# Performance work log

Hardware: AMD Instinct MI355X
Metric: run time of the kernel (lower is better)

Reference implementation:

```python
import jax, jax.numpy as jnp
import numpy as np

D = 2048          # hidden_size
N = 16            # num query heads
K = 8             # num kv heads
G = N // K        # GQA groups
H = 128           # head_dim (== head_dim_original, already padded)
T_NOISE = 1024
T_PAD = 1024
MAX_KV = 4096
THETA = 1000000.0
EPS = 1e-6
SM_SCALE = H ** -0.5
NEG = -1e30


def apply_rope(x, pos):
    # x: (T, heads, H); rotate-half (NeoX/Qwen) convention over full head_dim
    half = H // 2
    inv_freq = 1.0 / (THETA ** (jnp.arange(half, dtype=jnp.float32) / half))
    ang = pos.astype(jnp.float32)[:, None] * inv_freq[None, :]      # (T, half)
    cos = jnp.cos(ang)[:, None, :]
    sin = jnp.sin(ang)[:, None, :]
    x1, x2 = x[..., :half], x[..., half:]
    return jnp.concatenate([x1 * cos - x2 * sin, x2 * cos + x1 * sin], axis=-1)


def rms_norm(x, scale):
    var = jnp.mean(jnp.square(x), axis=-1, keepdims=True)
    return x * jax.lax.rsqrt(var + EPS) * scale


def setup_inputs() -> dict:
    key = jax.random.key(0)
    ks = jax.random.split(key, 10)
    cache_len = 1024
    actual_ctx = 768
    u = lambda k, shape: jax.random.uniform(k, shape, jnp.float32) * 0.01  # nnx uniform init
    return {
        "x_noise": jax.random.normal(ks[0], (T_NOISE, D), jnp.float32),
        "target_hidden": jax.random.normal(ks[1], (T_PAD, D), jnp.float32),
        "noise_positions": jnp.arange(T_NOISE, dtype=jnp.int32) + cache_len + actual_ctx,
        "ctx_positions": jnp.arange(T_PAD, dtype=jnp.int32) + cache_len,
        "kv_cache_k": jax.random.normal(ks[2], (1, N, MAX_KV, H), jnp.float32),
        "kv_cache_v": jax.random.normal(ks[3], (1, N, MAX_KV, H), jnp.float32),
        "cache_len": cache_len,
        "actual_ctx_count": actual_ctx,
        "Wq": u(ks[4], (D, N, H)),
        "Wk": u(ks[5], (D, K, H)),
        "Wv": u(ks[6], (D, K, H)),
        "Wo": u(ks[7], (N, H, D)),
        "q_scale": u(ks[8], (H,)),
        "k_scale": u(ks[9], (H,)),
    }


def reference(x_noise, target_hidden, noise_positions, ctx_positions,
              kv_cache_k, kv_cache_v, cache_len, actual_ctx_count,
              Wq, Wk, Wv, Wo, q_scale, k_scale):
    T_noise = x_noise.shape[0]
    T_padded = target_hidden.shape[0]
    # Q projection + RMSNorm + RoPE
    q = jnp.einsum('td,dnh->tnh', x_noise, Wq)
    q = apply_rope(rms_norm(q, q_scale), noise_positions)              # (Tq, N, H)
    # K/V over [context, noise]
    x_new = jnp.concatenate([target_hidden, x_noise], axis=0)
    k_new = jnp.einsum('td,dkh->tkh', x_new, Wk)
    v_new = jnp.einsum('td,dkh->tkh', x_new, Wv)
    new_positions = jnp.concatenate([ctx_positions, noise_positions], axis=0)
    k_new = apply_rope(rms_norm(k_new, k_scale), new_positions)
    # GQA expand before cache write (matches original)
    if G > 1:
        k_new = jnp.repeat(k_new, G, axis=1)
        v_new = jnp.repeat(v_new, G, axis=1)
    # Phase A: masked context write at cache_len
    ctx_mask = (jnp.arange(T_padded) < actual_ctx_count)[:, None, None]
    k_ctx = jnp.where(ctx_mask, k_new[:T_padded], 0.0)
    v_ctx = jnp.where(ctx_mask, v_new[:T_padded], 0.0)
    to4d = lambda a: a.transpose(1, 0, 2)[None]                        # (1, N, T, H)
    kv_cache_k = jax.lax.dynamic_update_slice(kv_cache_k, to4d(k_ctx), (0, 0, cache_len, 0))
    kv_cache_v = jax.lax.dynamic_update_slice(kv_cache_v, to4d(v_ctx), (0, 0, cache_len, 0))
    # Phase B: noise write at cache_len + actual_ctx_count
    noise_start = cache_len + actual_ctx_count
    kv_cache_k = jax.lax.dynamic_update_slice(kv_cache_k, to4d(k_new[T_padded:]), (0, 0, noise_start, 0))
    kv_cache_v = jax.lax.dynamic_update_slice(kv_cache_v, to4d(v_new[T_padded:]), (0, 0, noise_start, 0))
    new_cache_len = noise_start + T_noise
    # Non-causal attention over full cache, padding masked (segment_ids semantics)
    kv_valid = jnp.arange(MAX_KV) < new_cache_len                      # (MAX_KV,)
    scores = jnp.einsum('qnh,nkh->nqk', q, kv_cache_k[0]) * SM_SCALE   # (N, Tq, MAX_KV)
    scores = jnp.where(kv_valid[None, None, :], scores, NEG)
    probs = jax.nn.softmax(scores, axis=-1)
    attn = jnp.einsum('nqk,nkh->qnh', probs, kv_cache_v[0])            # (Tq, N, H)
    output = jnp.einsum('qnh,nhd->qd', attn, Wo)                       # (Tq, D)
    return (output, kv_cache_k, kv_cache_v)
```

## Files before the change

### kernel.cpp

```cpp
#include <hip/hip_runtime.h>
#include <hip/hip_bf16.h>
#include <math.h>

#define D 2048
#define NH 16
#define KHD 8
#define HD 128
#define T_NOISE 1024
#define T_PAD 1024
#define MAX_KV 4096
#define SM_SCALE 0.08838834764831845f

typedef __attribute__((ext_vector_type(8))) short short8;
typedef __attribute__((ext_vector_type(4))) short short4v;
typedef __attribute__((ext_vector_type(4))) float f32x4;

__device__ __forceinline__ unsigned short f2bf(float f) {
    union { float f; unsigned u; } v; v.f = f;
    unsigned r = v.u + 0x7fff + ((v.u >> 16) & 1);
    return (unsigned short)(r >> 16);
}
__device__ __forceinline__ float bf2f(short s) {
    union { unsigned u; float f; } v; v.u = ((unsigned)(unsigned short)s) << 16;
    return v.f;
}
__device__ __forceinline__ void gload16(const void* g, void* l) {
    __builtin_amdgcn_global_load_lds(
        (const __attribute__((address_space(1))) unsigned int*)g,
        (__attribute__((address_space(3))) unsigned int*)l, 16, 0, 0);
}
__device__ __forceinline__ unsigned cvtpk(float lo, float hi) {
    unsigned r;
    asm("v_cvt_pk_bf16_f32 %0, %1, %2" : "=v"(r) : "v"(lo), "v"(hi));
    return r;
}

__global__ __launch_bounds__(256)
void prep_all(const float* __restrict__ target_hidden, const float* __restrict__ x_noise,
              short* __restrict__ xbf,
              const float* __restrict__ Wk, const float* __restrict__ Wv,
              const float* __restrict__ Wq,
              short* __restrict__ dK, short* __restrict__ dV, short* __restrict__ dQ) {
    const int bid = blockIdx.x;
    const int tid = threadIdx.x;
    if (bid < 2048) {
        int i = (bid * 256 + tid) * 8;
        const float* src = (i < 1024 * 2048) ? (target_hidden + i)
                                             : (x_noise + (i - 1024 * 2048));
        float4 f0 = *(const float4*)src;
        float4 f1 = *(const float4*)(src + 4);
        short8 s;
        s[0] = (short)f2bf(f0.x); s[1] = (short)f2bf(f0.y);
        s[2] = (short)f2bf(f0.z); s[3] = (short)f2bf(f0.w);
        s[4] = (short)f2bf(f1.x); s[5] = (short)f2bf(f1.y);
        s[6] = (short)f2bf(f1.z); s[7] = (short)f2bf(f1.w);
        *(short8*)(xbf + i) = s;
        return;
    }
    __shared__ short t[64][72];
    const float* W; short* Wt; int r0, c0, C;
    if (bid < 3072) {
        int j = bid - 2048;
        int bx = j & 15, by = j >> 4;
        const bool isV = by >= 32;
        W = isV ? Wv : Wk; Wt = isV ? dV : dK;
        r0 = (by & 31) * 64; c0 = bx * 64; C = 1024;
    } else {
        int j = bid - 3072;
        int bx = j & 31, by = j >> 5;
        W = Wq; Wt = dQ;
        r0 = by * 64; c0 = bx * 64; C = 2048;
    }
    int rl = tid >> 4, cl4 = (tid & 15) * 4;
    #pragma unroll
    for (int j = 0; j < 4; ++j) {
        int r = rl + j * 16;
        float4 f = *(const float4*)(W + (size_t)(r0 + r) * C + c0 + cl4);
        t[cl4 + 0][r] = (short)f2bf(f.x);
        t[cl4 + 1][r] = (short)f2bf(f.y);
        t[cl4 + 2][r] = (short)f2bf(f.z);
        t[cl4 + 3][r] = (short)f2bf(f.w);
    }
    __syncthreads();
    #pragma unroll
    for (int j = 0; j < 2; ++j) {
        int idx = tid + j * 256;
        int cr = idx >> 3, rc8 = (idx & 7) * 8;
        *(short8*)(Wt + (size_t)(c0 + cr) * 2048 + r0 + rc8) = *(const short8*)&t[cr][rc8];
    }
}

__global__ __launch_bounds__(256)
void conv_transpose(const float* __restrict__ W, short* __restrict__ Wt,
                    int R, int C) {
    __shared__ short t[64][72];
    int tid = threadIdx.x;
    int r0 = blockIdx.y * 64, c0 = blockIdx.x * 64;
    int rl = tid >> 4, cl4 = (tid & 15) * 4;
    #pragma unroll
    for (int j = 0; j < 4; ++j) {
        int r = rl + j * 16;
        float4 f = *(const float4*)(W + (size_t)(r0 + r) * C + c0 + cl4);
        t[cl4 + 0][r] = (short)f2bf(f.x);
        t[cl4 + 1][r] = (short)f2bf(f.y);
        t[cl4 + 2][r] = (short)f2bf(f.z);
        t[cl4 + 3][r] = (short)f2bf(f.w);
    }
    __syncthreads();
    #pragma unroll
    for (int j = 0; j < 2; ++j) {
        int idx = tid + j * 256;
        int cr = idx >> 3, rc8 = (idx & 7) * 8;
        *(short8*)(Wt + (size_t)(c0 + cr) * R + r0 + rc8) = *(const short8*)&t[cr][rc8];
    }
}

__global__ __launch_bounds__(256)
void gemm_qkv64(const short* __restrict__ xbf, const short* __restrict__ Btp,
                short* __restrict__ k_tmpb, short* __restrict__ v_tmpb,
                short* __restrict__ q_tmpb) {
    const int n0 = blockIdx.x * 128;
    const int m0 = blockIdx.y * 64;
    const bool isQ = (n0 >= 2048);
    if (isQ && m0 >= 1024) return;
    const short* A = xbf + (isQ ? (size_t)1024 * 2048 : 0);

    __shared__ __align__(16) short As[64 * 32];
    __shared__ __align__(16) short Bs[128 * 32];
    const int tid = threadIdx.x;
    const int w = tid >> 6, lane = tid & 63;
    const int g = lane >> 4, li = lane & 15;
    const int wr = w >> 1, wc = w & 1;

    f32x4 acc[2][4];
    #pragma unroll
    for (int mi = 0; mi < 2; ++mi)
        #pragma unroll
        for (int ni = 0; ni < 4; ++ni) {
            acc[mi][ni][0] = 0.f; acc[mi][ni][1] = 0.f;
            acc[mi][ni][2] = 0.f; acc[mi][ni][3] = 0.f;
        }

    for (int k0 = 0; k0 < 2048; k0 += 32) {
        {
            int idx = w * 64 + lane;
            int row = idx >> 2, slot = idx & 3;
            gload16(A + (size_t)(m0 + row) * 2048 + k0 + slot * 8,
                    (char*)As + (size_t)(w * 64) * 16);
        }
        #pragma unroll
        for (int i = 0; i < 2; ++i) {
            int idx = i * 256 + w * 64 + lane;
            int row = idx >> 2, slot = idx & 3;
            gload16(Btp + (size_t)(n0 + row) * 2048 + k0 + slot * 8,
                    (char*)Bs + (size_t)(i * 256 + w * 64) * 16);
        }
        __syncthreads();
        short8 af[2], bf[4];
        #pragma unroll
        for (int mi = 0; mi < 2; ++mi)
            af[mi] = *(const short8*)&As[(wr * 32 + mi * 16 + li) * 32 + g * 8];
        #pragma unroll
        for (int ni = 0; ni < 4; ++ni)
            bf[ni] = *(const short8*)&Bs[(wc * 64 + ni * 16 + li) * 32 + g * 8];
        #pragma unroll
        for (int mi = 0; mi < 2; ++mi)
            #pragma unroll
            for (int ni = 0; ni < 4; ++ni)
                acc[mi][ni] = __builtin_amdgcn_mfma_f32_16x16x32_bf16(
                    af[mi], bf[ni], acc[mi][ni], 0, 0, 0);
        __syncthreads();
    }
    short* cp; int cbase, ldc2;
    if (n0 < 1024)      { cp = k_tmpb; cbase = 0;    ldc2 = 1024; }
    else if (n0 < 2048) { cp = v_tmpb; cbase = 1024; ldc2 = 1024; }
    else                { cp = q_tmpb; cbase = 2048; ldc2 = 2048; }
    #pragma unroll
    for (int mi = 0; mi < 2; ++mi)
        #pragma unroll
        for (int ni = 0; ni < 4; ++ni) {
            int n = n0 + wc * 64 + ni * 16 + li - cbase;
            #pragma unroll
            for (int r = 0; r < 4; ++r) {
                int m = m0 + wr * 32 + mi * 16 + 4 * g + r;
                cp[(size_t)m * ldc2 + n] = (short)f2bf(acc[mi][ni][r]);
            }
        }
}

__global__ __launch_bounds__(256)
void gemm_o(const short* __restrict__ A, const short* __restrict__ Bt,
            float* __restrict__ C) {
    __shared__ __align__(16) short As[64 * 32];
    __shared__ __align__(16) short Bs[64 * 32];
    const int tid = threadIdx.x;
    const int w = tid >> 6, lane = tid & 63;
    const int g = lane >> 4, li = lane & 15;
    const int wr = w >> 1, wc = w & 1;
    const int m0 = blockIdx.y * 64, n0 = blockIdx.x * 64;

    f32x4 acc[2][2];
    #pragma unroll
    for (int mi = 0; mi < 2; ++mi)
        #pragma unroll
        for (int ni = 0; ni < 2; ++ni) {
            acc[mi][ni][0] = 0.f; acc[mi][ni][1] = 0.f;
            acc[mi][ni][2] = 0.f; acc[mi][ni][3] = 0.f;
        }

    for (int k0 = 0; k0 < 2048; k0 += 32) {
        int idx = w * 64 + lane;
        int row = idx >> 2, slot = idx & 3;
        gload16(A + (size_t)(m0 + row) * 2048 + k0 + slot * 8,
                (char*)As + (size_t)(w * 64) * 16);
        gload16(Bt + (size_t)(n0 + row) * 2048 + k0 + slot * 8,
                (char*)Bs + (size_t)(w * 64) * 16);
        __syncthreads();
        short8 af[2], bf[2];
        #pragma unroll
        for (int mi = 0; mi < 2; ++mi)
            af[mi] = *(const short8*)&As[(wr * 32 + mi * 16 + li) * 32 + g * 8];
        #pragma unroll
        for (int ni = 0; ni < 2; ++ni)
            bf[ni] = *(const short8*)&Bs[(wc * 32 + ni * 16 + li) * 32 + g * 8];
        #pragma unroll
        for (int mi = 0; mi < 2; ++mi)
            #pragma unroll
            for (int ni = 0; ni < 2; ++ni)
                acc[mi][ni] = __builtin_amdgcn_mfma_f32_16x16x32_bf16(
                    af[mi], bf[ni], acc[mi][ni], 0, 0, 0);
        __syncthreads();
    }
    #pragma unroll
    for (int mi = 0; mi < 2; ++mi)
        #pragma unroll
        for (int ni = 0; ni < 2; ++ni) {
            int n = n0 + wc * 32 + ni * 16 + li;
            #pragma unroll
            for (int r = 0; r < 4; ++r) {
                int m = m0 + wr * 32 + mi * 16 + 4 * g + r;
                C[(size_t)m * 2048 + n] = acc[mi][ni][r];
            }
        }
}

__global__ __launch_bounds__(256)
void rmsrope_wv(short* __restrict__ qx, short* __restrict__ kx,
                const int* __restrict__ noise_pos, const int* __restrict__ ctx_pos,
                const float* __restrict__ q_scale, const float* __restrict__ k_scale) {
    const int bid = blockIdx.x;
    const bool isK = bid >= 4096;
    const int row = ((isK ? bid - 4096 : bid) << 2) + (threadIdx.x >> 6);
    const int l = threadIdx.x & 63;
    short* x; int hpt, splitT; const int *pA, *pB; const float* scale; float post;
    if (isK) { x = kx; hpt = 8;  pA = ctx_pos;   pB = noise_pos; splitT = 1024; scale = k_scale; post = 1.0f; }
    else     { x = qx; hpt = 16; pA = noise_pos; pB = noise_pos; splitT = 2048; scale = q_scale; post = SM_SCALE; }
    short* xr = x + (size_t)row * HD;
    const float v0 = bf2f(xr[l]), v1 = bf2f(xr[l + 64]);
    float ss = v0 * v0 + v1 * v1;
    #pragma unroll
    for (int off = 1; off < 64; off <<= 1) ss += __shfl_xor(ss, off);
    const float inv = rsqrtf(ss * (1.0f / 128.0f) + 1e-6f);
    const float n0 = v0 * inv * scale[l];
    const float n1 = v1 * inv * scale[l + 64];
    const int t = row / hpt;
    const int pos = (t < splitT) ? pA[t] : pB[t - splitT];
    const float inv_freq = expf((float)l * (-13.815510557964274f / 64.0f));
    const float ang = (float)pos * inv_freq;
    const float c = cosf(ang), s = sinf(ang);
    xr[l]      = (short)f2bf((n0 * c - n1 * s) * post);
    xr[l + 64] = (short)f2bf((n1 * c + n0 * s) * post);
}

__global__ __launch_bounds__(256)
void cache_scatter2(const float* __restrict__ in_k, const float* __restrict__ in_v,
                    const short* __restrict__ k_tmpb, const short* __restrict__ v_tmpb,
                    float* __restrict__ out_k, float* __restrict__ out_v,
                    short* __restrict__ kbf, short* __restrict__ vbf,
                    const int* __restrict__ clp, const int* __restrict__ acp) {
    const int cache_len = clp[0], actx = acp[0];
    const int noise_start = cache_len + actx;
    const int new_len = noise_start + T_NOISE;
    int i = blockIdx.x * 256 + threadIdx.x;
    int n = i >> 16;
    int rem = i & 65535;
    int pos = rem >> 4;
    int h8 = (rem & 15) << 3;
    size_t co = ((size_t)(n * MAX_KV + pos)) * HD + h8;
    short8 ks8, vs8;
    if (pos >= cache_len && pos < new_len) {
        int tkn = (pos < noise_start) ? (pos - cache_len) : (T_PAD + (pos - noise_start));
        size_t so = ((size_t)(tkn * KHD + (n >> 1))) * HD + h8;
        ks8 = *(const short8*)(k_tmpb + so);
        vs8 = *(const short8*)(v_tmpb + so);
        float4 a, b;
        a.x = bf2f(ks8[0]); a.y = bf2f(ks8[1]); a.z = bf2f(ks8[2]); a.w = bf2f(ks8[3]);
        b.x = bf2f(ks8[4]); b.y = bf2f(ks8[5]); b.z = bf2f(ks8[6]); b.w = bf2f(ks8[7]);
        *(float4*)(out_k + co) = a; *(float4*)(out_k + co + 4) = b;
        a.x = bf2f(vs8[0]); a.y = bf2f(vs8[1]); a.z = bf2f(vs8[2]); a.w = bf2f(vs8[3]);
        b.x = bf2f(vs8[4]); b.y = bf2f(vs8[5]); b.z = bf2f(vs8[6]); b.w = bf2f(vs8[7]);
        *(float4*)(out_v + co) = a; *(float4*)(out_v + co + 4) = b;
    } else {
        float4 ka = *(const float4*)(in_k + co);
        float4 kb = *(const float4*)(in_k + co + 4);
        float4 va = *(const float4*)(in_v + co);
        float4 vb = *(const float4*)(in_v + co + 4);
        *(float4*)(out_k + co) = ka; *(float4*)(out_k + co + 4) = kb;
        *(float4*)(out_v + co) = va; *(float4*)(out_v + co + 4) = vb;
        ks8[0] = (short)f2bf(ka.x); ks8[1] = (short)f2bf(ka.y);
        ks8[2] = (short)f2bf(ka.z); ks8[3] = (short)f2bf(ka.w);
        ks8[4] = (short)f2bf(kb.x); ks8[5] = (short)f2bf(kb.y);
        ks8[6] = (short)f2bf(kb.z); ks8[7] = (short)f2bf(kb.w);
        vs8[0] = (short)f2bf(va.x); vs8[1] = (short)f2bf(va.y);
        vs8[2] = (short)f2bf(va.z); vs8[3] = (short)f2bf(va.w);
        vs8[4] = (short)f2bf(vb.x); vs8[5] = (short)f2bf(vb.y);
        vs8[6] = (short)f2bf(vb.z); vs8[7] = (short)f2bf(vb.w);
    }
    if (pos < new_len) {
        *(short8*)(kbf + co) = ks8;
        *(short8*)(vbf + co) = vs8;
    }
}

#define VBUF(b) ((b) * 16896)

__device__ __forceinline__ short4v tr_read(unsigned addr) {
    short4v d;
    asm volatile("ds_read_b64_tr_b16 %0, %1" : "=v"(d) : "v"(addr));
    return d;
}

__global__ __launch_bounds__(128, 2)
void attn_mfma(const short* __restrict__ qbf, const short* __restrict__ kbf,
               const short* __restrict__ vbf, short* __restrict__ opA,
               short* __restrict__ opB, float* __restrict__ mlpart,
               const int* __restrict__ clp, const int* __restrict__ acp) {
    __shared__ __align__(16) char smem[33792];
    const int tid  = threadIdx.x;
    const int w    = tid >> 6;
    const int lane = tid & 63;
    const int g    = lane >> 4;
    const int li   = lane & 15;
    const int bid  = blockIdx.x;
    const int head = 2 * (bid & 7) + ((bid >> 3) & 1);
    const int rest = bid >> 4;
    const int q0   = (rest & 15) * 64;
    const int kvs  = rest >> 4;
    const int new_len = clp[0] + acp[0] + T_NOISE;
    const int ntiles  = (new_len + 63) >> 6;
    const int ntq     = (ntiles + 3) >> 2;

    const short* kb_g = kbf + (size_t)head * MAX_KV * HD;
    const short* vb_g = vbf + (size_t)head * MAX_KV * HD;

    short8 qf[2][4];
    #pragma unroll
    for (int sub = 0; sub < 2; ++sub) {
        const short* qp = qbf + ((size_t)(q0 + w * 32 + sub * 16 + li) * NH + head) * HD;
        #pragma unroll
        for (int ks = 0; ks < 4; ++ks) qf[sub][ks] = *(const short8*)(qp + 32 * ks + 8 * g);
    }

    f32x4 acc[2][8];
    #pragma unroll
    for (int sub = 0; sub < 2; ++sub)
        #pragma unroll
        for (int n = 0; n < 8; ++n) {
            acc[sub][n][0] = 0.f; acc[sub][n][1] = 0.f;
            acc[sub][n][2] = 0.f; acc[sub][n][3] = 0.f;
        }
    float m[2], l[2];
    m[0] = -INFINITY; m[1] = -INFINITY; l[0] = 0.f; l[1] = 0.f;

    const int vrloc = 4 * (lane >> 3) + ((lane >> 1) & 3);
    const int vcof  = (lane & 1) * 8;

    auto STAGE = [&](int tt, int bb) {
        const int base = (kvs * ntq + tt) * 64;
        #pragma unroll
        for (int half = 0; half < 2; ++half)
            #pragma unroll
            for (int i2 = 0; i2 < 4; ++i2) {
                const int ht = w * 4 + i2;
                gload16(vb_g + ((size_t)(base + half * 32 + vrloc) << 7) + ht * 16 + vcof,
                        smem + VBUF(bb) + half * 8448 + ht * 1056);
            }
    };

    short8 kpre[16];
    auto KLOAD = [&](int tt) {
        const int kp0 = (kvs * ntq + tt) << 6;
        const short* kr = kb_g + ((size_t)(kp0 + li) << 7) + g * 8;
        #pragma unroll
        for (int ks = 0; ks < 4; ++ks)
            #pragma unroll
            for (int j = 0; j < 4; ++j)
                kpre[ks * 4 + j] = *(const short8*)(kr + (size_t)(j * 16) * HD + ks * 32);
    };

    auto mkfrag = [&](const float* pA, const float* pB) -> short8 {
        unsigned w0 = cvtpk(pA[0], pA[1]), w1 = cvtpk(pA[2], pA[3]);
        unsigned w2 = cvtpk(pB[0], pB[1]), w3 = cvtpk(pB[2], pB[3]);
        const bool lowg = (g < 2);
        unsigned a0 = lowg ? w2 : w0, a1 = lowg ? w3 : w1;
        unsigned r0 = __shfl_xor((int)a0, 32), r1 = __shfl_xor((int)a1, 32);
        unsigned o0 = lowg ? w0 : w2, o1 = lowg ? w1 : w3;
        const bool sendOwn = (g == 1 || g == 2);
        unsigned b0 = sendOwn ? o0 : r0, b1 = sendOwn ? o1 : r1;
        unsigned g0_ = __shfl_xor((int)b0, 16), g1_ = __shfl_xor((int)b1, 16);
        union { unsigned u[4]; short8 s; } pau;
        pau.u[0] = (g == 0) ? o0 : (g == 2) ? r0 : g0_;
        pau.u[1] = (g == 0) ? o1 : (g == 2) ? r1 : g1_;
        pau.u[2] = (g == 3) ? o0 : (g == 1) ? r0 : g0_;
        pau.u[3] = (g == 3) ? o1 : (g == 1) ? r1 : g1_;
        return pau.s;
    };

    KLOAD(0);
    STAGE(0, 0);
    __syncthreads();

    for (int t = 0; t < ntq; ++t) {
        const int b = t & 1;
        if (t + 1 < ntq) STAGE(t + 1, b ^ 1);
        const int pos0 = (kvs * ntq + t) << 6;
        f32x4 s[4][2];
        #pragma unroll
        for (int j = 0; j < 4; ++j)
            #pragma unroll
            for (int sub = 0; sub < 2; ++sub) {
                s[j][sub][0] = 0.f; s[j][sub][1] = 0.f;
                s[j][sub][2] = 0.f; s[j][sub][3] = 0.f;
            }
        #pragma unroll
        for (int ks = 0; ks < 4; ++ks)
            #pragma unroll
            for (int j = 0; j < 4; ++j) {
                short8 kf = kpre[ks * 4 + j];
                s[j][0] = __builtin_amdgcn_mfma_f32_16x16x32_bf16(kf, qf[0][ks], s[j][0], 0, 0, 0);
                s[j][1] = __builtin_amdgcn_mfma_f32_16x16x32_bf16(kf, qf[1][ks], s[j][1], 0, 0, 0);
            }
        if (t + 1 < ntq) KLOAD(t + 1);
        #pragma unroll
        for (int j = 0; j < 4; ++j)
            #pragma unroll
            for (int r = 0; r < 4; ++r)
                if (pos0 + 16 * j + 4 * g + r >= new_len) {
                    s[j][0][r] = -1e30f; s[j][1][r] = -1e30f;
                }
        short8 pa[2][2];
        #pragma unroll
        for (int sub = 0; sub < 2; ++sub) {
            float tm = -INFINITY;
            #pragma unroll
            for (int j = 0; j < 4; ++j)
                #pragma unroll
                for (int r = 0; r < 4; ++r) tm = fmaxf(tm, s[j][sub][r]);
            tm = fmaxf(tm, __shfl_xor(tm, 16));
            tm = fmaxf(tm, __shfl_xor(tm, 32));
            if (tm > m[sub] + 8.f) {
                const float alpha = __expf(m[sub] - tm);
                m[sub] = tm;
                l[sub] *= alpha;
                #pragma unroll
                for (int n = 0; n < 8; ++n) {
                    acc[sub][n][0] *= alpha; acc[sub][n][1] *= alpha;
                    acc[sub][n][2] *= alpha; acc[sub][n][3] *= alpha;
                }
            }
            const float mb = m[sub];
            float p[4][4];
            float rs = 0.f;
            #pragma unroll
            for (int j = 0; j < 4; ++j)
                #pragma unroll
                for (int r = 0; r < 4; ++r) {
                    p[j][r] = __expf(s[j][sub][r] - mb);
                    rs += p[j][r];
                }
            rs += __shfl_xor(rs, 16);
            rs += __shfl_xor(rs, 32);
            l[sub] += rs;
            pa[sub][0] = mkfrag(p[0], p[1]);
            pa[sub][1] = mkfrag(p[2], p[3]);
        }
        #pragma unroll
        for (int half = 0; half < 2; ++half) {
            const unsigned vb0 = (unsigned)(size_t)(smem + VBUF(b)) + half * 8448
                               + g * 256 + li * 8;
            short4v vt[16];
            #pragma unroll
            for (int h2 = 0; h2 < 8; ++h2) {
                vt[2 * h2]     = tr_read(vb0 + h2 * 1056);
                vt[2 * h2 + 1] = tr_read(vb0 + h2 * 1056 + 128);
            }
            asm volatile("s_waitcnt lgkmcnt(0)" ::: "memory");
            __builtin_amdgcn_sched_barrier(0);
            #pragma unroll
            for (int h2 = 0; h2 < 8; ++h2) {
                short8 vf = __builtin_shufflevector(vt[2 * h2], vt[2 * h2 + 1],
                                                    0, 1, 2, 3, 4, 5, 6, 7);
                acc[0][h2] = __builtin_amdgcn_mfma_f32_16x16x32_bf16(vf, pa[0][half], acc[0][h2], 0, 0, 0);
                acc[1][h2] = __builtin_amdgcn_mfma_f32_16x16x32_bf16(vf, pa[1][half], acc[1][h2], 0, 0, 0);
            }
        }
        __syncthreads();
    }

    short* op = (kvs < 2) ? (opA + (size_t)kvs * 16 * 1024 * 128)
                          : (opB + (size_t)(kvs - 2) * 16 * 1024 * 128);
    #pragma unroll
    for (int sub = 0; sub < 2; ++sub) {
        const int qrow = q0 + w * 32 + sub * 16 + li;
        const size_t ro = ((size_t)(head << 10) + qrow) * 128;
        #pragma unroll
        for (int n = 0; n < 8; ++n) {
            short4v o4;
            o4[0] = (short)f2bf(acc[sub][n][0]); o4[1] = (short)f2bf(acc[sub][n][1]);
            o4[2] = (short)f2bf(acc[sub][n][2]); o4[3] = (short)f2bf(acc[sub][n][3]);
            *(short4v*)(op + ro + 16 * n + 4 * g) = o4;
        }
        if (g == 0) {
            float* ml = mlpart + (((size_t)(kvs * 16 + head) << 10) + qrow) * 2;
            ml[0] = m[sub]; ml[1] = l[sub];
        }
    }
}

__global__ __launch_bounds__(256)
void attn_merge(const short* __restrict__ opA, const short* __restrict__ opB,
                const float* __restrict__ mlpart, short* __restrict__ a_bf) {
    int gid = blockIdx.x * 256 + threadIdx.x;
    int row = gid >> 4;
    int c8  = (gid & 15) * 8;
    int head = row >> 10, q = row & 1023;
    float mg[4], lg[4], mstar = -INFINITY;
    #pragma unroll
    for (int s = 0; s < 4; ++s) {
        const float* ml = mlpart + (((size_t)(s * 16 + head) << 10) + q) * 2;
        mg[s] = ml[0]; lg[s] = ml[1];
        mstar = fmaxf(mstar, mg[s]);
    }
    float cg[4], lstar = 0.f;
    #pragma unroll
    for (int s = 0; s < 4; ++s) { cg[s] = __expf(mg[s] - mstar); lstar += lg[s] * cg[s]; }
    const float inv = 1.0f / lstar;
    float o[8] = {};
    #pragma unroll
    for (int s = 0; s < 4; ++s) {
        const short* op = (s < 2) ? (opA + (size_t)s * 16 * 1024 * 128)
                                  : (opB + (size_t)(s - 2) * 16 * 1024 * 128);
        short8 v = *(const short8*)(op + (((size_t)(head << 10)) + q) * 128 + c8);
        #pragma unroll
        for (int j = 0; j < 8; ++j) o[j] += cg[s] * bf2f(v[j]);
    }
    short8 o8;
    #pragma unroll
    for (int j = 0; j < 8; ++j) o8[j] = (short)f2bf(o[j] * inv);
    *(short8*)(a_bf + (size_t)q * 2048 + head * 128 + c8) = o8;
}

extern "C" void kernel_launch(void* const* d_in, const int* in_sizes, int n_in,
                              void* d_out, int out_size, void* d_ws, size_t ws_size,
                              hipStream_t stream) {
    const float* x_noise       = (const float*)d_in[0];
    const float* target_hidden = (const float*)d_in[1];
    const int*   noise_pos     = (const int*)d_in[2];
    const int*   ctx_pos       = (const int*)d_in[3];
    const float* in_k          = (const float*)d_in[4];
    const float* in_v          = (const float*)d_in[5];
    const int*   clp           = (const int*)d_in[6];
    const int*   acp           = (const int*)d_in[7];
    const float* Wq            = (const float*)d_in[8];
    const float* Wk            = (const float*)d_in[9];
    const float* Wv            = (const float*)d_in[10];
    const float* Wo            = (const float*)d_in[11];
    const float* q_scale       = (const float*)d_in[12];
    const float* k_scale       = (const float*)d_in[13];

    float* out   = (float*)d_out;
    float* out_k = out + (size_t)T_NOISE * D;
    float* out_v = out_k + (size_t)NH * MAX_KV * HD;

    float* ws     = (float*)d_ws;
    const size_t M1 = 1024u * 1024u;
    short* q_tmpb = (short*)ws;
    short* a_bf   = q_tmpb;
    short* k_tmpb = (short*)(ws + 1 * M1);
    short* v_tmpb = (short*)(ws + 2 * M1);
    float* mlpart = (float*)v_tmpb;
    short* xbf    = (short*)(ws + 3 * M1);
    short* opartA = xbf;
    short* btpack = (short*)(ws + 5 * M1);
    short* wo_t   = btpack;
    short* opartB = (short*)(ws + 7 * M1);
    short* kbf    = (short*)(ws + 9 * M1);
    short* vbf    = (short*)(ws + 13 * M1);

    dim3 blk(256);
    prep_all<<<4096, blk, 0, stream>>>(target_hidden, x_noise, xbf,
                                       Wk, Wv, Wq,
                                       btpack, btpack + (size_t)1024 * 2048,
                                       btpack + (size_t)2048 * 2048);
    gemm_qkv64<<<dim3(32, 32), blk, 0, stream>>>(xbf, btpack, k_tmpb, v_tmpb, q_tmpb);
    conv_transpose<<<dim3(32, 32), blk, 0, stream>>>(Wo, wo_t, 2048, 2048);
    rmsrope_wv<<<8192, blk, 0, stream>>>(q_tmpb, k_tmpb, noise_pos, ctx_pos,
                                         q_scale, k_scale);
    cache_scatter2<<<4096, blk, 0, stream>>>(in_k, in_v, k_tmpb, v_tmpb,
                                             out_k, out_v, kbf, vbf, clp, acp);
    attn_mfma<<<1024, 128, 0, stream>>>(q_tmpb, kbf, vbf, opartA, opartB, mlpart, clp, acp);
    attn_merge<<<1024, blk, 0, stream>>>(opartA, opartB, mlpart, a_bf);
    gemm_o<<<dim3(32, 16), blk, 0, stream>>>(a_bf, wo_t, out);
}
```

Before: 197.3 us.

## Split attention KV range six ways, drop double buffering for higher occupancy

Raises the flash-decoding style KV split from 4 to 6 partitions, giving 1536 attention blocks instead of 1024. The V stage becomes single-buffered (half the LDS) and K fragments are loaded inline rather than prefetched into registers, so launch bounds can go to 3 blocks per SIMD. It also adds an early exit for tiles past the valid length, and the merge kernel now reduces 6 partials. The trade is more partial outputs to merge and lost load/compute overlap inside each block, in exchange for more parallelism and occupancy.

```diff
diff --git a/kernel.cpp b/kernel.cpp
--- a/kernel.cpp
+++ b/kernel.cpp
@@ -9,6 +9,7 @@
 #define T_NOISE 1024
 #define T_PAD 1024
 #define MAX_KV 4096
+#define NSPLIT 6
 #define SM_SCALE 0.08838834764831845f
 
 typedef __attribute__((ext_vector_type(8))) short short8;
@@ -322,20 +323,21 @@
     }
 }
 
-#define VBUF(b) ((b) * 16896)
-
 __device__ __forceinline__ short4v tr_read(unsigned addr) {
     short4v d;
     asm volatile("ds_read_b64_tr_b16 %0, %1" : "=v"(d) : "v"(addr));
     return d;
 }
 
-__global__ __launch_bounds__(128, 2)
+__global__ __launch_bounds__(128, 3)
 void attn_mfma(const short* __restrict__ qbf, const short* __restrict__ kbf,
-               const short* __restrict__ vbf, short* __restrict__ opA,
-               short* __restrict__ opB, float* __restrict__ mlpart,
+               const short* __restrict__ vbf,
+               short* __restrict__ op0, short* __restrict__ op1,
+               short* __restrict__ op2, short* __restrict__ op3,
+               short* __restrict__ op4, short* __restrict__ op5,
+               float* __restrict__ mlpart,
                const int* __restrict__ clp, const int* __restrict__ acp) {
-    __shared__ __align__(16) char smem[33792];
+    __shared__ __align__(16) char smem[16896];
     const int tid  = threadIdx.x;
     const int w    = tid >> 6;
     const int lane = tid & 63;
@@ -348,7 +350,7 @@
     const int kvs  = rest >> 4;
     const int new_len = clp[0] + acp[0] + T_NOISE;
     const int ntiles  = (new_len + 63) >> 6;
-    const int ntq     = (ntiles + 3) >> 2;
+    const int ntq     = (ntiles + NSPLIT - 1) / NSPLIT;
 
     const short* kb_g = kbf + (size_t)head * MAX_KV * HD;
     const short* vb_g = vbf + (size_t)head * MAX_KV * HD;
@@ -375,7 +377,7 @@
     const int vrloc = 4 * (lane >> 3) + ((lane >> 1) & 3);
     const int vcof  = (lane & 1) * 8;
 
-    auto STAGE = [&](int tt, int bb) {
+    auto STAGE = [&](int tt) {
         const int base = (kvs * ntq + tt) * 64;
         #pragma unroll
         for (int half = 0; half < 2; ++half)
@@ -383,19 +385,8 @@
             for (int i2 = 0; i2 < 4; ++i2) {
                 const int ht = w * 4 + i2;
                 gload16(vb_g + ((size_t)(base + half * 32 + vrloc) << 7) + ht * 16 + vcof,
-                        smem + VBUF(bb) + half * 8448 + ht * 1056);
+                        smem + half * 8448 + ht * 1056);
             }
-    };
-
-    short8 kpre[16];
-    auto KLOAD = [&](int tt) {
-        const int kp0 = (kvs * ntq + tt) << 6;
-        const short* kr = kb_g + ((size_t)(kp0 + li) << 7) + g * 8;
-        #pragma unroll
-        for (int ks = 0; ks < 4; ++ks)
-            #pragma unroll
-            for (int j = 0; j < 4; ++j)
-                kpre[ks * 4 + j] = *(const short8*)(kr + (size_t)(j * 16) * HD + ks * 32);
     };
 
     auto mkfrag = [&](const float* pA, const float* pB) -> short8 {
@@ -416,14 +407,10 @@
         return pau.s;
     };
 
-    KLOAD(0);
-    STAGE(0, 0);
-    __syncthreads();
-
     for (int t = 0; t < ntq; ++t) {
-        const int b = t & 1;
-        if (t + 1 < ntq) STAGE(t + 1, b ^ 1);
         const int pos0 = (kvs * ntq + t) << 6;
+        if (pos0 >= new_len) break;
+        STAGE(t);
         f32x4 s[4][2];
         #pragma unroll
         for (int j = 0; j < 4; ++j)
@@ -432,15 +419,17 @@
                 s[j][sub][0] = 0.f; s[j][sub][1] = 0.f;
                 s[j][sub][2] = 0.f; s[j][sub][3] = 0.f;
             }
-        #pragma unroll
-        for (int ks = 0; ks < 4; ++ks)
-            #pragma unroll
-            for (int j = 0; j < 4; ++j) {
-                short8 kf = kpre[ks * 4 + j];
-                s[j][0] = __builtin_amdgcn_mfma_f32_16x16x32_bf16(kf, qf[0][ks], s[j][0], 0, 0, 0);
-                s[j][1] = __builtin_amdgcn_mfma_f32_16x16x32_bf16(kf, qf[1][ks], s[j][1], 0, 0, 0);
-            }
-        if (t + 1 < ntq) KLOAD(t + 1);
+        {
+            const short* kr = kb_g + ((size_t)(pos0 + li) << 7) + g * 8;
+            #pragma unroll
+            for (int ks = 0; ks < 4; ++ks)
+                #pragma unroll
+                for (int j = 0; j < 4; ++j) {
+                    short8 kf = *(const short8*)(kr + (size_t)(j * 16) * HD + ks * 32);
+                    s[j][0] = __builtin_amdgcn_mfma_f32_16x16x32_bf16(kf, qf[0][ks], s[j][0], 0, 0, 0);
+                    s[j][1] = __builtin_amdgcn_mfma_f32_16x16x32_bf16(kf, qf[1][ks], s[j][1], 0, 0, 0);
+                }
+        }
         #pragma unroll
         for (int j = 0; j < 4; ++j)
             #pragma unroll
@@ -484,9 +473,10 @@
             pa[sub][0] = mkfrag(p[0], p[1]);
             pa[sub][1] = mkfrag(p[2], p[3]);
         }
+        __syncthreads();
         #pragma unroll
         for (int half = 0; half < 2; ++half) {
-            const unsigned vb0 = (unsigned)(size_t)(smem + VBUF(b)) + half * 8448
+            const unsigned vb0 = (unsigned)(size_t)smem + half * 8448
                                + g * 256 + li * 8;
             short4v vt[16];
             #pragma unroll
@@ -507,8 +497,8 @@
         __syncthreads();
     }
 
-    short* op = (kvs < 2) ? (opA + (size_t)kvs * 16 * 1024 * 128)
-                          : (opB + (size_t)(kvs - 2) * 16 * 1024 * 128);
+    short* op = (kvs == 0) ? op0 : (kvs == 1) ? op1 : (kvs == 2) ? op2
+              : (kvs == 3) ? op3 : (kvs == 4) ? op4 : op5;
     #pragma unroll
     for (int sub = 0; sub < 2; ++sub) {
         const int qrow = q0 + w * 32 + sub * 16 + li;
@@ -528,29 +518,30 @@
 }
 
 __global__ __launch_bounds__(256)
-void attn_merge(const short* __restrict__ opA, const short* __restrict__ opB,
+void attn_merge(const short* __restrict__ op0, const short* __restrict__ op1,
+                const short* __restrict__ op2, const short* __restrict__ op3,
+                const short* __restrict__ op4, const short* __restrict__ op5,
                 const float* __restrict__ mlpart, short* __restrict__ a_bf) {
+    const short* ops[NSPLIT] = {op0, op1, op2, op3, op4, op5};
     int gid = blockIdx.x * 256 + threadIdx.x;
     int row = gid >> 4;
     int c8  = (gid & 15) * 8;
     int head = row >> 10, q = row & 1023;
-    float mg[4], lg[4], mstar = -INFINITY;
-    #pragma unroll
-    for (int s = 0; s < 4; ++s) {
+    float mg[NSPLIT], lg[NSPLIT], mstar = -INFINITY;
+    #pragma unroll
+    for (int s = 0; s < NSPLIT; ++s) {
         const float* ml = mlpart + (((size_t)(s * 16 + head) << 10) + q) * 2;
         mg[s] = ml[0]; lg[s] = ml[1];
         mstar = fmaxf(mstar, mg[s]);
     }
-    float cg[4], lstar = 0.f;
-    #pragma unroll
-    for (int s = 0; s < 4; ++s) { cg[s] = __expf(mg[s] - mstar); lstar += lg[s] * cg[s]; }
+    float cg[NSPLIT], lstar = 0.f;
+    #pragma unroll
+    for (int s = 0; s < NSPLIT; ++s) { cg[s] = __expf(mg[s] - mstar); lstar += lg[s] * cg[s]; }
     const float inv = 1.0f / lstar;
     float o[8] = {};
     #pragma unroll
-    for (int s = 0; s < 4; ++s) {
-        const short* op = (s < 2) ? (opA + (size_t)s * 16 * 1024 * 128)
-                                  : (opB + (size_t)(s - 2) * 16 * 1024 * 128);
-        short8 v = *(const short8*)(op + (((size_t)(head << 10)) + q) * 128 + c8);
+    for (int s = 0; s < NSPLIT; ++s) {
+        short8 v = *(const short8*)(ops[s] + (((size_t)(head << 10)) + q) * 128 + c8);
         #pragma unroll
         for (int j = 0; j < 8; ++j) o[j] += cg[s] * bf2f(v[j]);
     }
@@ -588,14 +579,18 @@
     short* a_bf   = q_tmpb;
     short* k_tmpb = (short*)(ws + 1 * M1);
     short* v_tmpb = (short*)(ws + 2 * M1);
-    float* mlpart = (float*)v_tmpb;
+    float* mlpart = (float*)(ws + 2 * M1);
     short* xbf    = (short*)(ws + 3 * M1);
-    short* opartA = xbf;
     short* btpack = (short*)(ws + 5 * M1);
     short* wo_t   = btpack;
-    short* opartB = (short*)(ws + 7 * M1);
     short* kbf    = (short*)(ws + 9 * M1);
     short* vbf    = (short*)(ws + 13 * M1);
+    short* op0 = k_tmpb;
+    short* op1 = xbf;
+    short* op2 = (short*)(ws + 4 * M1);
+    short* op3 = (short*)(ws + 7 * M1);
+    short* op4 = (short*)(ws + 8 * M1);
+    short* op5 = (short*)out;
 
     dim3 blk(256);
     prep_all<<<4096, blk, 0, stream>>>(target_hidden, x_noise, xbf,
@@ -608,7 +603,8 @@
                                          q_scale, k_scale);
     cache_scatter2<<<4096, blk, 0, stream>>>(in_k, in_v, k_tmpb, v_tmpb,
                                              out_k, out_v, kbf, vbf, clp, acp);
-    attn_mfma<<<1024, 128, 0, stream>>>(q_tmpb, kbf, vbf, opartA, opartB, mlpart, clp, acp);
-    attn_merge<<<1024, blk, 0, stream>>>(opartA, opartB, mlpart, a_bf);
+    attn_mfma<<<16 * 16 * NSPLIT, 128, 0, stream>>>(
+        q_tmpb, kbf, vbf, op0, op1, op2, op3, op4, op5, mlpart, clp, acp);
+    attn_merge<<<1024, blk, 0, stream>>>(op0, op1, op2, op3, op4, op5, mlpart, a_bf);
     gemm_o<<<dim3(32, 16), blk, 0, stream>>>(a_bf, wo_t, out);
 }
```

Result: slower. 209.7 us (+6.3%).
